# Kernel optimization log

Hardware: AMD Instinct MI355X
Metric: run time of the kernel (lower is better)

The kernel has to match this reference:

```python
import jax, jax.numpy as jnp
import numpy as np

N_NODES = 100000
N_EDGES = 1200000
MAX_ATOM_TYPE = 100
NUM_FEATURES = 92
GC_DIM = 64          # pre_layer_dim == gc_dim == CGConv channels
NUM_RBF = 32
NUM_GC_LAYERS = 4
CUTOFF_UPPER = 5.0
BN_EPS = 1e-5


def setup_inputs() -> dict:
    key = jax.random.key(0)
    ks = jax.random.split(key, 12)
    atom_types = jax.random.randint(ks[0], (N_NODES,), 0, MAX_ATOM_TYPE, dtype=jnp.int32)
    pos = jax.random.uniform(ks[1], (N_NODES, 3), dtype=jnp.float32) * 6.0  # box side 6 -> many dists < cutoff
    edge_index = jax.random.randint(ks[2], (2, N_EDGES), 0, N_NODES, dtype=jnp.int32)
    # parameters
    emb = jax.random.normal(ks[3], (MAX_ATOM_TYPE, NUM_FEATURES), dtype=jnp.float32)
    s = 1.0 / np.sqrt(NUM_FEATURES)
    pre_W = jax.random.uniform(ks[4], (NUM_FEATURES, GC_DIM), minval=-s, maxval=s, dtype=jnp.float32)
    pre_b = jnp.zeros((GC_DIM,), jnp.float32)
    zdim = 2 * GC_DIM + NUM_RBF  # [x_i, x_j, edge_attr]
    sz = 1.0 / np.sqrt(zdim)
    Wf = jax.random.uniform(ks[5], (NUM_GC_LAYERS, zdim, GC_DIM), minval=-sz, maxval=sz, dtype=jnp.float32)
    bf = jnp.zeros((NUM_GC_LAYERS, GC_DIM), jnp.float32)
    Ws = jax.random.uniform(ks[6], (NUM_GC_LAYERS, zdim, GC_DIM), minval=-sz, maxval=sz, dtype=jnp.float32)
    bs = jnp.zeros((NUM_GC_LAYERS, GC_DIM), jnp.float32)
    bn_gamma = jnp.ones((NUM_GC_LAYERS, GC_DIM), jnp.float32)
    bn_beta = jnp.zeros((NUM_GC_LAYERS, GC_DIM), jnp.float32)
    # ExpNormalSmearing (torchmd-net) init
    start = np.exp(-CUTOFF_UPPER)
    means = jnp.asarray(np.linspace(start, 1.0, NUM_RBF), jnp.float32)
    betas = jnp.full((NUM_RBF,), (2.0 / NUM_RBF * (1.0 - start)) ** -2, jnp.float32)
    return {"atom_types": atom_types, "pos": pos, "edge_index": edge_index,
            "emb": emb, "pre_W": pre_W, "pre_b": pre_b,
            "Wf": Wf, "bf": bf, "Ws": Ws, "bs": bs,
            "bn_gamma": bn_gamma, "bn_beta": bn_beta,
            "means": means, "betas": betas}


def _forward(atom_types, pos, edge_index, emb, pre_W, pre_b, Wf, bf, Ws, bs,
             bn_gamma, bn_beta, means, betas):
    src, dst = edge_index[0], edge_index[1]
    # distance (edge_vec = pos[src] - pos[dst])
    vec = pos[src] - pos[dst]                                  # [E,3]
    dist = jnp.sqrt(jnp.sum(vec * vec, axis=-1) + 1e-12)       # [E]
    # expnorm RBF with cosine cutoff (cutoff_lower = 0)
    cutoff = 0.5 * (jnp.cos(dist * (np.pi / CUTOFF_UPPER)) + 1.0) * (dist < CUTOFF_UPPER)
    alpha = 5.0 / CUTOFF_UPPER
    edge_attr = cutoff[:, None] * jnp.exp(
        -betas * (jnp.exp(-alpha * dist)[:, None] - means) ** 2)  # [E,NUM_RBF]
    # embedding + pre layer
    x = emb[atom_types]                                        # [N,F]
    x = jax.nn.relu(x @ pre_W + pre_b)                         # [N,C]
    # mean-aggregation degree (scatter-mean denominator)
    deg = jax.ops.segment_sum(jnp.ones_like(dist), dst, num_segments=N_NODES)
    inv_deg = jnp.where(deg > 0, 1.0 / jnp.maximum(deg, 1.0), 0.0)[:, None]
    for l in range(NUM_GC_LAYERS):
        # CGConv: z = [x_i, x_j, e]; out = x + mean_j(sigmoid(lin_f(z)) * softplus(lin_s(z)))
        z = jnp.concatenate([x[dst], x[src], edge_attr], axis=-1)   # [E, 2C+R]
        msg = jax.nn.sigmoid(z @ Wf[l] + bf[l]) * jax.nn.softplus(z @ Ws[l] + bs[l])
        agg = jax.ops.segment_sum(msg, dst, num_segments=N_NODES) * inv_deg
        x = x + agg
        # BatchNorm1d (batch statistics, biased var, as in torch training mode)
        mu = jnp.mean(x, axis=0)
        var = jnp.mean((x - mu) ** 2, axis=0)
        x = (x - mu) * jax.lax.rsqrt(var + BN_EPS) * bn_gamma[l] + bn_beta[l]
    return x


def reference(atom_types, pos, edge_index, emb, pre_W, pre_b, Wf, bf, Ws, bs,
              bn_gamma, bn_beta, means, betas):
    return _forward(atom_types, pos, edge_index, emb, pre_W, pre_b, Wf, bf, Ws, bs,
                    bn_gamma, bn_beta, means, betas)
```

## Files before the change

### kernel.cpp

```cpp
#include <hip/hip_runtime.h>
#include <math.h>

#define N_NODES 100000
#define N_EDGES 1200000
#define GC 64
#define RBF 32
#define NLAYERS 4
#define NF 92
#define NATOM 100
#define BN_EPS 1e-5f
#define TILE_GRID 2048
#define NWIN (N_EDGES / 16)
#define LOG2E 1.44269504f
#define LN2 0.69314718f

typedef _Float16 half8 __attribute__((ext_vector_type(8)));
typedef _Float16 half4 __attribute__((ext_vector_type(4)));
typedef _Float16 half2v __attribute__((ext_vector_type(2)));
typedef float f32x4 __attribute__((ext_vector_type(4)));
union U32H2 { unsigned int u; half2v h; };

__global__ __launch_bounds__(256) void deg_kernel(
    const int* __restrict__ ei, int* __restrict__ deg)
{
    int e = blockIdx.x * 256 + threadIdx.x;
    if (e >= N_EDGES) return;
    atomicAdd(&deg[ei[N_EDGES + e]], 1);
}

__global__ __launch_bounds__(256) void scan_a_kernel(const int* __restrict__ deg, int* __restrict__ bsums)
{
    __shared__ int sm[256];
    int tid = threadIdx.x;
    int i = blockIdx.x * 256 + tid;
    int v = (i < N_NODES) ? deg[i] : 0;
    sm[tid] = v;
    __syncthreads();
    for (int s = 128; s > 0; s >>= 1) {
        if (tid < s) sm[tid] += sm[tid + s];
        __syncthreads();
    }
    if (tid == 0) bsums[blockIdx.x] = sm[0];
}

__global__ __launch_bounds__(512) void scan_b_kernel(const int* __restrict__ bsums, int* __restrict__ boffs)
{
    __shared__ int sm[512];
    int tid = threadIdx.x;
    int v = (tid < 391) ? bsums[tid] : 0;
    sm[tid] = v;
    __syncthreads();
    for (int off = 1; off < 512; off <<= 1) {
        int t = (tid >= off) ? sm[tid - off] : 0;
        __syncthreads();
        sm[tid] += t;
        __syncthreads();
    }
    boffs[tid] = (tid == 0) ? 0 : sm[tid - 1];
}

__global__ __launch_bounds__(256) void scan_c_kernel(
    const int* __restrict__ deg, const int* __restrict__ boffs,
    int* __restrict__ row_st, float* __restrict__ inv_deg)
{
    __shared__ int sm[256];
    int tid = threadIdx.x;
    int i = blockIdx.x * 256 + tid;
    int v = (i < N_NODES) ? deg[i] : 0;
    sm[tid] = v;
    __syncthreads();
    for (int off = 1; off < 256; off <<= 1) {
        int t = (tid >= off) ? sm[tid - off] : 0;
        __syncthreads();
        sm[tid] += t;
        __syncthreads();
    }
    if (i <= N_NODES) row_st[i] = boffs[blockIdx.x] + sm[tid] - v;
    if (i < N_NODES) inv_deg[i] = (v > 0) ? (1.0f / (float)v) : 0.0f;
}

__global__ __launch_bounds__(256) void scatter_perm_kernel(
    const int* __restrict__ ei, const int* __restrict__ row_st,
    int* __restrict__ cursor, int2* __restrict__ csr_sd)
{
    int e = blockIdx.x * 256 + threadIdx.x;
    if (e >= N_EDGES) return;
    int s = ei[e];
    int d = ei[N_EDGES + e];
    int p = atomicAdd(&cursor[d], 1);
    csr_sd[row_st[d] + p] = make_int2(s, d);
}

__global__ __launch_bounds__(256) void edge_post_kernel(
    const int2* __restrict__ csr_sd, const float* __restrict__ pos,
    const float* __restrict__ inv_deg,
    const float* __restrict__ means, const float* __restrict__ betas,
    int* __restrict__ csr_src, int* __restrict__ csr_dst,
    unsigned int* __restrict__ ea,
    unsigned char* __restrict__ seg8, int* __restrict__ wnode,
    _Float16* __restrict__ inv_e)
{
    __shared__ int sdst[256];
    int t = blockIdx.x * 256 + threadIdx.x;
    if (t < N_EDGES) {
        int2 v = csr_sd[t];
        int s = v.x, d = v.y;
        csr_src[t] = s;
        csr_dst[t] = d;
        sdst[threadIdx.x] = d;
        inv_e[t] = (_Float16)(inv_deg[d] * LN2);

        float dx = pos[s * 3 + 0] - pos[d * 3 + 0];
        float dy = pos[s * 3 + 1] - pos[d * 3 + 1];
        float dz = pos[s * 3 + 2] - pos[d * 3 + 2];
        float dist = sqrtf(dx * dx + dy * dy + dz * dz + 1e-12f);
        float cut = 0.0f;
        if (dist < 5.0f) cut = 0.5f * (__cosf(dist * 0.6283185307179586f) + 1.0f);
        float ex = __expf(-dist);
        union { _Float16 h[32]; uint4 u[4]; } pk;
#pragma unroll
        for (int k = 0; k < 32; k++) {
            float vk = ex - means[k];
            pk.h[k] = (_Float16)(cut * __expf(-betas[k] * vk * vk));
        }
        uint4* op = (uint4*)(ea + (size_t)t * 16);
        op[0] = pk.u[0];
        op[1] = pk.u[1];
        op[2] = pk.u[2];
        op[3] = pk.u[3];
    }
    __syncthreads();
    if (threadIdx.x < 16) {
        int w0 = blockIdx.x * 16 + threadIdx.x;
        if ((size_t)w0 * 16 < N_EDGES) {
            int lb = threadIdx.x * 16;
            int gb = w0 * 16;
            int prev = -1, sg = -1;
            for (int k = 0; k < 16; k++) {
                int dd = sdst[lb + k];
                if (dd != prev) { sg++; prev = dd; wnode[gb + sg] = dd; }
                seg8[gb + k] = (unsigned char)sg;
            }
            for (int m = sg + 1; m < 16; m++) wnode[gb + m] = -1;
        }
    }
}

__global__ __launch_bounds__(256) void prep_const_kernel(
    const float* __restrict__ Wf, const float* __restrict__ Ws,
    _Float16* __restrict__ wf16, _Float16* __restrict__ ws16,
    const float* __restrict__ emb, const float* __restrict__ pre_W,
    const float* __restrict__ pre_b, float* __restrict__ T)
{
    int b = blockIdx.x;
    if (b < 160) {
        int i = b * 256 + threadIdx.x;
        int l = i / (160 * GC);
        int r = i - l * 160 * GC;
        int k = r >> 6;
        int col = r & 63;
        size_t o = ((size_t)l * GC + col) * 160 + k;
        wf16[o] = (_Float16)(Wf[i] * LOG2E);
        ws16[o] = (_Float16)(Ws[i] * LOG2E);
    } else {
        int a = (b - 160) * 4 + (threadIdx.x >> 6);
        int c = threadIdx.x & 63;
        if (a < NATOM) {
            float acc = pre_b[c];
            for (int k = 0; k < NF; k++) acc = fmaf(emb[a * NF + k], pre_W[k * GC + c], acc);
            T[a * GC + c] = fmaxf(acc, 0.0f);
        }
    }
}

static __device__ __forceinline__ void proj_mfma16(
    const _Float16* __restrict__ wf, const _Float16* __restrict__ ws,
    const float* __restrict__ bfv, const float* __restrict__ bsv,
    const half8 Bn[2], int cb, int node, unsigned int* __restrict__ P2u)
{
    const int lane = threadIdx.x & 63;
    const int quad = lane >> 4;
    const int r16 = lane & 15;
    f32x4 accf[2], accs[2];
#pragma unroll
    for (int sub = 0; sub < 2; sub++) {
        accf[sub] = (f32x4){0.f, 0.f, 0.f, 0.f};
        accs[sub] = (f32x4){0.f, 0.f, 0.f, 0.f};
    }
#pragma unroll
    for (int kt = 0; kt < 2; kt++) {
#pragma unroll
        for (int sub = 0; sub < 2; sub++) {
            int chan = cb + sub * 16 + r16;
            half8 a = *(const half8*)(wf + (size_t)chan * 160 + kt * 32 + quad * 8);
            half8 b = *(const half8*)(ws + (size_t)chan * 160 + kt * 32 + quad * 8);
            accf[sub] = __builtin_amdgcn_mfma_f32_16x16x32_f16(a, Bn[kt], accf[sub], 0, 0, 0);
            accs[sub] = __builtin_amdgcn_mfma_f32_16x16x32_f16(b, Bn[kt], accs[sub], 0, 0, 0);
        }
    }
#pragma unroll
    for (int sub = 0; sub < 2; sub++) {
        float4 bf4 = *(const float4*)(bfv + cb + sub * 16 + quad * 4);
        float4 bs4 = *(const float4*)(bsv + cb + sub * 16 + quad * 4);
        half8 h = { (_Float16)(accf[sub][0] + bf4.x * LOG2E), (_Float16)(accs[sub][0] + bs4.x * LOG2E),
                    (_Float16)(accf[sub][1] + bf4.y * LOG2E), (_Float16)(accs[sub][1] + bs4.y * LOG2E),
                    (_Float16)(accf[sub][2] + bf4.z * LOG2E), (_Float16)(accs[sub][2] + bs4.z * LOG2E),
                    (_Float16)(accf[sub][3] + bf4.w * LOG2E), (_Float16)(accs[sub][3] + bs4.w * LOG2E) };
        *(half8*)(P2u + (size_t)node * GC + cb + sub * 16 + quad * 4) = h;
    }
}

__global__ __launch_bounds__(256) void initproj_kernel(
    const int* __restrict__ atom_types, const float* __restrict__ T,
    float* __restrict__ x, _Float16* __restrict__ x16,
    const _Float16* __restrict__ wf, const _Float16* __restrict__ ws,
    const float* __restrict__ bfv, const float* __restrict__ bsv,
    unsigned int* __restrict__ P2u)
{
    __shared__ _Float16 lx[32 * 72];
    const int nb = blockIdx.x * 32;

#pragma unroll
    for (int rep = 0; rep < 2; rep++) {
        int g = rep * 256 + threadIdx.x;
        int gi = blockIdx.x * 512 + g;
        int node = g >> 4;
        int c4 = (g & 15) * 4;
        int a = atom_types[nb + node];
        float4 v = ((const float4*)T)[a * 16 + (g & 15)];
        ((float4*)x)[gi] = v;
        half4 h = { (_Float16)v.x, (_Float16)v.y, (_Float16)v.z, (_Float16)v.w };
        ((half4*)x16)[gi] = h;
        *(half4*)(lx + node * 72 + c4) = h;
    }
    __syncthreads();

    const int lane = threadIdx.x & 63;
    const int wid = threadIdx.x >> 6;
    const int quad = lane >> 4;
    const int r16 = lane & 15;
    const int cb = (wid & 1) * 32;
    const int tn = (wid >> 1) * 16 + r16;
    half8 Bn[2];
    Bn[0] = *(const half8*)(lx + tn * 72 + quad * 8);
    Bn[1] = *(const half8*)(lx + tn * 72 + 32 + quad * 8);
    proj_mfma16(wf, ws, bfv, bsv, Bn, cb, nb + tn, P2u);
}

__global__ __launch_bounds__(256) void bnproj_kernel(
    const float* __restrict__ xn, const float* __restrict__ stats,
    const float* __restrict__ gamma, const float* __restrict__ beta,
    float* __restrict__ xout, _Float16* __restrict__ x16,
    const _Float16* __restrict__ wf, const _Float16* __restrict__ ws,
    const float* __restrict__ bfv, const float* __restrict__ bsv,
    unsigned int* __restrict__ P2u)
{
    __shared__ _Float16 lx[32 * 72];
    const int nb = blockIdx.x * 32;
    const float invN = 1.0f / (float)N_NODES;

#pragma unroll
    for (int rep = 0; rep < 2; rep++) {
        int g = rep * 256 + threadIdx.x;
        int gi = blockIdx.x * 512 + g;
        int node = g >> 4;
        int c4 = (g & 15) * 4;
        float4 v = ((const float4*)xn)[gi];
        float vv[4] = {v.x, v.y, v.z, v.w};
        float o[4];
#pragma unroll
        for (int t = 0; t < 4; t++) {
            int c = c4 + t;
            float mu = stats[c] * invN;
            float var = stats[64 + c] * invN - mu * mu;
            float sc = gamma[c] * rsqrtf(var + BN_EPS);
            o[t] = (vv[t] - mu) * sc + beta[c];
        }
        ((float4*)xout)[gi] = make_float4(o[0], o[1], o[2], o[3]);
        half4 h = { (_Float16)o[0], (_Float16)o[1], (_Float16)o[2], (_Float16)o[3] };
        ((half4*)x16)[gi] = h;
        *(half4*)(lx + node * 72 + c4) = h;
    }
    __syncthreads();

    const int lane = threadIdx.x & 63;
    const int wid = threadIdx.x >> 6;
    const int quad = lane >> 4;
    const int r16 = lane & 15;
    const int cb = (wid & 1) * 32;
    const int tn = (wid >> 1) * 16 + r16;
    half8 Bn[2];
    Bn[0] = *(const half8*)(lx + tn * 72 + quad * 8);
    Bn[1] = *(const half8*)(lx + tn * 72 + 32 + quad * 8);
    proj_mfma16(wf, ws, bfv, bsv, Bn, cb, nb + tn, P2u);
}

static __device__ __forceinline__ void compute_win(
    half8 S0, half8 S1, half8 E, int4 d4, int moff,
    const half8 (&WGF)[3][2], const half8 (&WGS)[3][2],
    int r16, int quad, int cb,
    const unsigned char* __restrict__ seg8, const int* __restrict__ wnode,
    const _Float16* __restrict__ inv_e, const unsigned int* __restrict__ P2u,
    float* __restrict__ x)
{
    unsigned int pv0, pv1, pv2, pv3, pv4, pv5, pv6, pv7;
    {
        const unsigned int* p0 = P2u + (size_t)d4.x * GC + cb + r16;
        const unsigned int* p1 = P2u + (size_t)d4.y * GC + cb + r16;
        const unsigned int* p2 = P2u + (size_t)d4.z * GC + cb + r16;
        const unsigned int* p3 = P2u + (size_t)d4.w * GC + cb + r16;
        pv0 = p0[0];  pv4 = p0[16];
        pv1 = p1[0];  pv5 = p1[16];
        pv2 = p2[0];  pv6 = p2[16];
        pv3 = p3[0];  pv7 = p3[16];
    }
    unsigned int segq = *(const unsigned int*)(seg8 + moff + quad * 4);
    int4 wn4 = *(const int4*)(wnode + moff + quad * 4);
    half4 inv4 = *(const half4*)(inv_e + moff + quad * 4);

    const f32x4 zf = (f32x4){0.0f, 0.0f, 0.0f, 0.0f};
    f32x4 accf[2], accs[2];
    __builtin_amdgcn_s_setprio(1);
#pragma unroll
    for (int ctl = 0; ctl < 2; ctl++) {
        accf[ctl] = __builtin_amdgcn_mfma_f32_16x16x32_f16(S0, WGF[0][ctl], zf, 0, 0, 0);
        accs[ctl] = __builtin_amdgcn_mfma_f32_16x16x32_f16(S0, WGS[0][ctl], zf, 0, 0, 0);
        accf[ctl] = __builtin_amdgcn_mfma_f32_16x16x32_f16(S1, WGF[1][ctl], accf[ctl], 0, 0, 0);
        accs[ctl] = __builtin_amdgcn_mfma_f32_16x16x32_f16(S1, WGS[1][ctl], accs[ctl], 0, 0, 0);
        accf[ctl] = __builtin_amdgcn_mfma_f32_16x16x32_f16(E,  WGF[2][ctl], accf[ctl], 0, 0, 0);
        accs[ctl] = __builtin_amdgcn_mfma_f32_16x16x32_f16(E,  WGS[2][ctl], accs[ctl], 0, 0, 0);
    }
    __builtin_amdgcn_s_setprio(0);

    unsigned int pvv[8] = {pv0, pv1, pv2, pv3, pv4, pv5, pv6, pv7};
    half4 msgh[2];
#pragma unroll
    for (int ctl = 0; ctl < 2; ctl++) {
#pragma unroll
        for (int rr = 0; rr < 4; rr++) {
            U32H2 t; t.u = pvv[ctl * 4 + rr];
            float af = accf[ctl][rr] + (float)t.h.x;
            float as = accs[ctl][rr] + (float)t.h.y;
            float sg = __builtin_amdgcn_rcpf(1.0f + __builtin_amdgcn_exp2f(-af));
            float sp = __builtin_amdgcn_logf(1.0f + __builtin_amdgcn_exp2f(as));
            msgh[ctl][rr] = (_Float16)(sg * sp);
        }
    }
    half4 am;
#pragma unroll
    for (int j = 0; j < 4; j++) {
        int sj = (segq >> (8 * j)) & 0xff;
        am[j] = (sj == r16) ? inv4[j] : (_Float16)0.0f;
    }
    int wa[4] = { wn4.x, wn4.y, wn4.z, wn4.w };
#pragma unroll
    for (int ctl = 0; ctl < 2; ctl++) {
        f32x4 red = __builtin_amdgcn_mfma_f32_16x16x16f16(am, msgh[ctl], zf, 0, 0, 0);
#pragma unroll
        for (int rr = 0; rr < 4; rr++) {
            int nd = wa[rr];
            if (nd >= 0) atomicAdd(&x[(size_t)nd * GC + cb + ctl * 16 + r16], red[rr]);
        }
    }
}

#define LOADSET(S0_, S1_, EE_, SRC_, WW_)                                            \
    S0_ = *(const half8*)(x16 + (size_t)(SRC_) * GC + quad * 8);                     \
    S1_ = *(const half8*)(x16 + (size_t)(SRC_) * GC + 32 + quad * 8);                \
    EE_ = *(const half8*)(ea + ((size_t)(WW_) * 16 + r16) * RBF + quad * 8);

__global__ __launch_bounds__(256, 3) void win_mfma_kernel(
    const _Float16* __restrict__ x16, const _Float16* __restrict__ ea,
    const int* __restrict__ csr_src, const int* __restrict__ csr_dst,
    const unsigned char* __restrict__ seg8, const int* __restrict__ wnode,
    const _Float16* __restrict__ inv_e, const unsigned int* __restrict__ P2u,
    const _Float16* __restrict__ wf16, const _Float16* __restrict__ ws16,
    float* __restrict__ x)
{
    const int lane = threadIdx.x & 63;
    const int wid = __builtin_amdgcn_readfirstlane(threadIdx.x >> 6);
    const int quad = lane >> 4;
    const int r16 = lane & 15;
    const int wgid = blockIdx.x * 4 + wid;
    const int cb = (wgid & 1) * 32;
    int w = wgid >> 1;
    const int NSEQ = TILE_GRID * 2;

    half8 WGF[3][2], WGS[3][2];
#pragma unroll
    for (int ctl = 0; ctl < 2; ctl++) {
        const _Float16* wfp = wf16 + (size_t)(cb + ctl * 16 + r16) * 160 + 64 + quad * 8;
        const _Float16* wsp = ws16 + (size_t)(cb + ctl * 16 + r16) * 160 + 64 + quad * 8;
#pragma unroll
        for (int kt = 0; kt < 3; kt++) {
            WGF[kt][ctl] = *(const half8*)(wfp + kt * 32);
            WGS[kt][ctl] = *(const half8*)(wsp + kt * 32);
        }
    }

    half8 AS0, AS1, AE, BS0, BS1, BE, CS0, CS1, CE;
    int4 d4A, d4B, d4C;
    int moffA, moffB, moffC;
    {
        int s_ = csr_src[w * 16 + r16];
        d4A = *(const int4*)(csr_dst + w * 16 + quad * 4);
        LOADSET(AS0, AS1, AE, s_, w);
        moffA = w * 16;
    }
    {
        int wB = w + NSEQ; if (wB >= NWIN) wB = NWIN - 1;
        int s_ = csr_src[wB * 16 + r16];
        d4B = *(const int4*)(csr_dst + wB * 16 + quad * 4);
        LOADSET(BS0, BS1, BE, s_, wB);
        moffB = wB * 16;
    }
    {
        int wCx = w + 2 * NSEQ; if (wCx >= NWIN) wCx = NWIN - 1;
        int s_ = csr_src[wCx * 16 + r16];
        d4C = *(const int4*)(csr_dst + wCx * 16 + quad * 4);
        LOADSET(CS0, CS1, CE, s_, wCx);
        moffC = wCx * 16;
    }
    int wD = w + 3 * NSEQ; if (wD >= NWIN) wD = NWIN - 1;
    int sD = csr_src[wD * 16 + r16];
    int4 d4D = *(const int4*)(csr_dst + wD * 16 + quad * 4);

    while (true) {
        compute_win(AS0, AS1, AE, d4A, moffA,
                    WGF, WGS, r16, quad, cb, seg8, wnode, inv_e, P2u, x);
        LOADSET(AS0, AS1, AE, sD, wD);
        d4A = d4D; moffA = wD * 16;
        wD += NSEQ; if (wD >= NWIN) wD = NWIN - 1;
        sD = csr_src[wD * 16 + r16];
        d4D = *(const int4*)(csr_dst + wD * 16 + quad * 4);
        w += NSEQ;
        if (w >= NWIN) break;

        compute_win(BS0, BS1, BE, d4B, moffB,
                    WGF, WGS, r16, quad, cb, seg8, wnode, inv_e, P2u, x);
        LOADSET(BS0, BS1, BE, sD, wD);
        d4B = d4D; moffB = wD * 16;
        wD += NSEQ; if (wD >= NWIN) wD = NWIN - 1;
        sD = csr_src[wD * 16 + r16];
        d4D = *(const int4*)(csr_dst + wD * 16 + quad * 4);
        w += NSEQ;
        if (w >= NWIN) break;

        compute_win(CS0, CS1, CE, d4C, moffC,
                    WGF, WGS, r16, quad, cb, seg8, wnode, inv_e, P2u, x);
        LOADSET(CS0, CS1, CE, sD, wD);
        d4C = d4D; moffC = wD * 16;
        wD += NSEQ; if (wD >= NWIN) wD = NWIN - 1;
        sD = csr_src[wD * 16 + r16];
        d4D = *(const int4*)(csr_dst + wD * 16 + quad * 4);
        w += NSEQ;
        if (w >= NWIN) break;
    }
}

__global__ __launch_bounds__(256) void stats_kernel(const float* __restrict__ x, float* __restrict__ stats)
{
    const int lane = threadIdx.x & 63;
    const int wid = threadIdx.x >> 6;
    int w = blockIdx.x * 4 + wid;
    float s1 = 0.0f, s2 = 0.0f;
    for (int n = w; n < N_NODES; n += 2048) {
        float v = x[(size_t)n * GC + lane];
        s1 += v;
        s2 = fmaf(v, v, s2);
    }
    __shared__ float rs1[4][64];
    __shared__ float rs2[4][64];
    rs1[wid][lane] = s1;
    rs2[wid][lane] = s2;
    __syncthreads();
    if (threadIdx.x < 64) {
        atomicAdd(&stats[lane], rs1[0][lane] + rs1[1][lane] + rs1[2][lane] + rs1[3][lane]);
    } else if (threadIdx.x < 128) {
        int c = threadIdx.x & 63;
        atomicAdd(&stats[64 + c], rs2[0][c] + rs2[1][c] + rs2[2][c] + rs2[3][c]);
    }
}

__global__ __launch_bounds__(256) void bn_kernel(
    const float* __restrict__ xn, const float* __restrict__ stats,
    const float* __restrict__ gamma, const float* __restrict__ beta,
    float* __restrict__ out)
{
    int i = blockIdx.x * 256 + threadIdx.x;
    int c4 = (i & 15) * 4;
    float4 v = ((const float4*)xn)[i];
    float vv[4] = {v.x, v.y, v.z, v.w};
    float o[4];
    const float invN = 1.0f / (float)N_NODES;
#pragma unroll
    for (int t = 0; t < 4; t++) {
        int c = c4 + t;
        float mu = stats[c] * invN;
        float var = stats[64 + c] * invN - mu * mu;
        float sc = gamma[c] * rsqrtf(var + BN_EPS);
        o[t] = (vv[t] - mu) * sc + beta[c];
    }
    ((float4*)out)[i] = make_float4(o[0], o[1], o[2], o[3]);
}

extern "C" void kernel_launch(void* const* d_in, const int* in_sizes, int n_in,
                              void* d_out, int out_size, void* d_ws, size_t ws_size,
                              hipStream_t stream)
{
    const int* atom_types = (const int*)d_in[0];
    const float* pos = (const float*)d_in[1];
    const int* edge_index = (const int*)d_in[2];
    const float* emb = (const float*)d_in[3];
    const float* pre_W = (const float*)d_in[4];
    const float* pre_b = (const float*)d_in[5];
    const float* Wf = (const float*)d_in[6];
    const float* bf = (const float*)d_in[7];
    const float* Ws = (const float*)d_in[8];
    const float* bs = (const float*)d_in[9];
    const float* gamma = (const float*)d_in[10];
    const float* beta = (const float*)d_in[11];
    const float* means = (const float*)d_in[12];
    const float* betas = (const float*)d_in[13];

    char* base = (char*)d_ws;
    char* p = base;
    auto alloc = [&](size_t bytes) -> char* {
        char* r = p;
        p += (bytes + 255) & ~(size_t)255;
        return r;
    };
    unsigned int* ea = (unsigned int*)alloc((size_t)N_EDGES * RBF * 2);
    float* x = (float*)alloc((size_t)N_NODES * GC * 4);
    _Float16* x16 = (_Float16*)alloc((size_t)N_NODES * GC * 2);
    unsigned int* P2u = (unsigned int*)alloc((size_t)N_NODES * GC * 4);
    int2* csr_sd = (int2*)alloc((size_t)N_EDGES * 8);
    int* csr_src = (int*)alloc((size_t)N_EDGES * 4);
    int* csr_dst = (int*)alloc((size_t)N_EDGES * 4);
    int* wnode = (int*)alloc((size_t)N_EDGES * 4);
    unsigned char* seg8 = (unsigned char*)alloc((size_t)N_EDGES);
    _Float16* inv_e = (_Float16*)alloc((size_t)N_EDGES * 2);
    _Float16* wf16 = (_Float16*)alloc((size_t)NLAYERS * GC * 160 * 2);
    _Float16* ws16 = (_Float16*)alloc((size_t)NLAYERS * GC * 160 * 2);
    int* row_st = (int*)alloc((size_t)(N_NODES + 1) * 4);
    float* inv_deg = (float*)alloc((size_t)N_NODES * 4);
    float* T = (float*)alloc((size_t)NATOM * GC * 4);
    int* bsums = (int*)alloc(512 * 4);
    int* boffs = (int*)alloc(512 * 4);
    const size_t ZR_INTS = (size_t)2 * N_NODES + 128 * NLAYERS + 64;
    char* zr = alloc(ZR_INTS * 4);
    int* deg = (int*)zr;
    int* cursor = deg + N_NODES;
    float* stats = (float*)(cursor + N_NODES);

    if ((size_t)(p - base) > ws_size) return;

    (void)hipMemsetAsync(zr, 0, ZR_INTS * 4, stream);

    const int EG = (N_EDGES + 255) / 256;
    deg_kernel<<<EG, 256, 0, stream>>>(edge_index, deg);
    scan_a_kernel<<<391, 256, 0, stream>>>(deg, bsums);
    scan_b_kernel<<<1, 512, 0, stream>>>(bsums, boffs);
    scan_c_kernel<<<391, 256, 0, stream>>>(deg, boffs, row_st, inv_deg);
    scatter_perm_kernel<<<EG, 256, 0, stream>>>(edge_index, row_st, cursor, csr_sd);
    edge_post_kernel<<<EG, 256, 0, stream>>>(csr_sd, pos, inv_deg, means, betas,
                                             csr_src, csr_dst, ea, seg8, wnode, inv_e);
    prep_const_kernel<<<185, 256, 0, stream>>>(Wf, Ws, wf16, ws16, emb, pre_W, pre_b, T);
    initproj_kernel<<<N_NODES / 32, 256, 0, stream>>>(atom_types, T, x, x16,
                                                      wf16, ws16, bf, bs, P2u);

    for (int l = 0; l < NLAYERS; l++) {
        win_mfma_kernel<<<TILE_GRID, 256, 0, stream>>>(
            x16, (const _Float16*)ea, csr_src, csr_dst, seg8, wnode, inv_e, P2u,
            wf16 + (size_t)l * GC * 160, ws16 + (size_t)l * GC * 160, x);
        stats_kernel<<<512, 256, 0, stream>>>(x, stats + l * 128);
        if (l < NLAYERS - 1) {
            bnproj_kernel<<<N_NODES / 32, 256, 0, stream>>>(
                x, stats + l * 128, gamma + l * GC, beta + l * GC, x, x16,
                wf16 + (size_t)(l + 1) * GC * 160, ws16 + (size_t)(l + 1) * GC * 160,
                bf + (l + 1) * GC, bs + (l + 1) * GC, P2u);
        } else {
            bn_kernel<<<N_NODES * 16 / 256, 256, 0, stream>>>(
                x, stats + l * 128, gamma + l * GC, beta + l * GC, (float*)d_out);
        }
    }
}
```

Baseline: 801.0 us.

## Capture atomic rank in degree pass, fold block-offset scan, use nontemporal loads

The degree kernel now records each edge's atomic return value as its rank within its destination. The scatter step then places edges directly into csr_src/csr_dst with no second atomic pass and no intermediate int2 buffer. The separate single-block offset scan is removed; each scan_c block sums its preceding block totals itself. Streaming edge data in the main message-passing kernel (ea, csr indices, seg8, wnode, inv_e) is read with nontemporal loads so it does not push reused node data out of cache. Costs are an extra rank array and redundant prefix reductions in every scan block.

```diff
diff --git a/kernel.cpp b/kernel.cpp
--- a/kernel.cpp
+++ b/kernel.cpp
@@ -18,14 +18,15 @@
 typedef _Float16 half4 __attribute__((ext_vector_type(4)));
 typedef _Float16 half2v __attribute__((ext_vector_type(2)));
 typedef float f32x4 __attribute__((ext_vector_type(4)));
+typedef int i32x4 __attribute__((ext_vector_type(4)));
 union U32H2 { unsigned int u; half2v h; };
 
-__global__ __launch_bounds__(256) void deg_kernel(
-    const int* __restrict__ ei, int* __restrict__ deg)
+__global__ __launch_bounds__(256) void degrank_kernel(
+    const int* __restrict__ ei, int* __restrict__ deg, int* __restrict__ rank)
 {
     int e = blockIdx.x * 256 + threadIdx.x;
     if (e >= N_EDGES) return;
-    atomicAdd(&deg[ei[N_EDGES + e]], 1);
+    rank[e] = atomicAdd(&deg[ei[N_EDGES + e]], 1);
 }
 
 __global__ __launch_bounds__(256) void scan_a_kernel(const int* __restrict__ deg, int* __restrict__ bsums)
@@ -43,28 +44,24 @@
     if (tid == 0) bsums[blockIdx.x] = sm[0];
 }
 
-__global__ __launch_bounds__(512) void scan_b_kernel(const int* __restrict__ bsums, int* __restrict__ boffs)
-{
-    __shared__ int sm[512];
-    int tid = threadIdx.x;
-    int v = (tid < 391) ? bsums[tid] : 0;
-    sm[tid] = v;
-    __syncthreads();
-    for (int off = 1; off < 512; off <<= 1) {
-        int t = (tid >= off) ? sm[tid - off] : 0;
-        __syncthreads();
-        sm[tid] += t;
-        __syncthreads();
-    }
-    boffs[tid] = (tid == 0) ? 0 : sm[tid - 1];
-}
-
 __global__ __launch_bounds__(256) void scan_c_kernel(
-    const int* __restrict__ deg, const int* __restrict__ boffs,
+    const int* __restrict__ deg, const int* __restrict__ bsums,
     int* __restrict__ row_st, float* __restrict__ inv_deg)
 {
     __shared__ int sm[256];
     int tid = threadIdx.x;
+    int acc = 0;
+    if (tid < blockIdx.x) acc = bsums[tid];
+    int t2 = tid + 256;
+    if (t2 < blockIdx.x) acc += bsums[t2];
+    sm[tid] = acc;
+    __syncthreads();
+    for (int s = 128; s > 0; s >>= 1) {
+        if (tid < s) sm[tid] += sm[tid + s];
+        __syncthreads();
+    }
+    int boff = sm[0];
+    __syncthreads();
     int i = blockIdx.x * 256 + tid;
     int v = (i < N_NODES) ? deg[i] : 0;
     sm[tid] = v;
@@ -75,27 +72,27 @@
         sm[tid] += t;
         __syncthreads();
     }
-    if (i <= N_NODES) row_st[i] = boffs[blockIdx.x] + sm[tid] - v;
+    if (i <= N_NODES) row_st[i] = boff + sm[tid] - v;
     if (i < N_NODES) inv_deg[i] = (v > 0) ? (1.0f / (float)v) : 0.0f;
 }
 
 __global__ __launch_bounds__(256) void scatter_perm_kernel(
     const int* __restrict__ ei, const int* __restrict__ row_st,
-    int* __restrict__ cursor, int2* __restrict__ csr_sd)
+    const int* __restrict__ rank, int* __restrict__ csr_src, int* __restrict__ csr_dst)
 {
     int e = blockIdx.x * 256 + threadIdx.x;
     if (e >= N_EDGES) return;
     int s = ei[e];
     int d = ei[N_EDGES + e];
-    int p = atomicAdd(&cursor[d], 1);
-    csr_sd[row_st[d] + p] = make_int2(s, d);
+    int idx = row_st[d] + rank[e];
+    csr_src[idx] = s;
+    csr_dst[idx] = d;
 }
 
 __global__ __launch_bounds__(256) void edge_post_kernel(
-    const int2* __restrict__ csr_sd, const float* __restrict__ pos,
-    const float* __restrict__ inv_deg,
+    const int* __restrict__ csr_src, const int* __restrict__ csr_dst,
+    const float* __restrict__ pos, const float* __restrict__ inv_deg,
     const float* __restrict__ means, const float* __restrict__ betas,
-    int* __restrict__ csr_src, int* __restrict__ csr_dst,
     unsigned int* __restrict__ ea,
     unsigned char* __restrict__ seg8, int* __restrict__ wnode,
     _Float16* __restrict__ inv_e)
@@ -103,10 +100,8 @@
     __shared__ int sdst[256];
     int t = blockIdx.x * 256 + threadIdx.x;
     if (t < N_EDGES) {
-        int2 v = csr_sd[t];
-        int s = v.x, d = v.y;
-        csr_src[t] = s;
-        csr_dst[t] = d;
+        int s = csr_src[t];
+        int d = csr_dst[t];
         sdst[threadIdx.x] = d;
         inv_e[t] = (_Float16)(inv_deg[d] * LN2);
 
@@ -296,7 +291,7 @@
 }
 
 static __device__ __forceinline__ void compute_win(
-    half8 S0, half8 S1, half8 E, int4 d4, int moff,
+    half8 S0, half8 S1, half8 E, i32x4 d4, int moff,
     const half8 (&WGF)[3][2], const half8 (&WGS)[3][2],
     int r16, int quad, int cb,
     const unsigned char* __restrict__ seg8, const int* __restrict__ wnode,
@@ -305,18 +300,18 @@
 {
     unsigned int pv0, pv1, pv2, pv3, pv4, pv5, pv6, pv7;
     {
-        const unsigned int* p0 = P2u + (size_t)d4.x * GC + cb + r16;
-        const unsigned int* p1 = P2u + (size_t)d4.y * GC + cb + r16;
-        const unsigned int* p2 = P2u + (size_t)d4.z * GC + cb + r16;
-        const unsigned int* p3 = P2u + (size_t)d4.w * GC + cb + r16;
+        const unsigned int* p0 = P2u + (size_t)d4[0] * GC + cb + r16;
+        const unsigned int* p1 = P2u + (size_t)d4[1] * GC + cb + r16;
+        const unsigned int* p2 = P2u + (size_t)d4[2] * GC + cb + r16;
+        const unsigned int* p3 = P2u + (size_t)d4[3] * GC + cb + r16;
         pv0 = p0[0];  pv4 = p0[16];
         pv1 = p1[0];  pv5 = p1[16];
         pv2 = p2[0];  pv6 = p2[16];
         pv3 = p3[0];  pv7 = p3[16];
     }
-    unsigned int segq = *(const unsigned int*)(seg8 + moff + quad * 4);
-    int4 wn4 = *(const int4*)(wnode + moff + quad * 4);
-    half4 inv4 = *(const half4*)(inv_e + moff + quad * 4);
+    unsigned int segq = __builtin_nontemporal_load((const unsigned int*)(seg8 + moff + quad * 4));
+    i32x4 wn4 = __builtin_nontemporal_load((const i32x4*)(wnode + moff + quad * 4));
+    half4 inv4 = __builtin_nontemporal_load((const half4*)(inv_e + moff + quad * 4));
 
     const f32x4 zf = (f32x4){0.0f, 0.0f, 0.0f, 0.0f};
     f32x4 accf[2], accs[2];
@@ -352,13 +347,12 @@
         int sj = (segq >> (8 * j)) & 0xff;
         am[j] = (sj == r16) ? inv4[j] : (_Float16)0.0f;
     }
-    int wa[4] = { wn4.x, wn4.y, wn4.z, wn4.w };
 #pragma unroll
     for (int ctl = 0; ctl < 2; ctl++) {
         f32x4 red = __builtin_amdgcn_mfma_f32_16x16x16f16(am, msgh[ctl], zf, 0, 0, 0);
 #pragma unroll
         for (int rr = 0; rr < 4; rr++) {
-            int nd = wa[rr];
+            int nd = wn4[rr];
             if (nd >= 0) atomicAdd(&x[(size_t)nd * GC + cb + ctl * 16 + r16], red[rr]);
         }
     }
@@ -367,7 +361,7 @@
 #define LOADSET(S0_, S1_, EE_, SRC_, WW_)                                            \
     S0_ = *(const half8*)(x16 + (size_t)(SRC_) * GC + quad * 8);                     \
     S1_ = *(const half8*)(x16 + (size_t)(SRC_) * GC + 32 + quad * 8);                \
-    EE_ = *(const half8*)(ea + ((size_t)(WW_) * 16 + r16) * RBF + quad * 8);
+    EE_ = __builtin_nontemporal_load((const half8*)(ea + ((size_t)(WW_) * 16 + r16) * RBF + quad * 8));
 
 __global__ __launch_bounds__(256, 3) void win_mfma_kernel(
     const _Float16* __restrict__ x16, const _Float16* __restrict__ ea,
@@ -399,31 +393,31 @@
     }
 
     half8 AS0, AS1, AE, BS0, BS1, BE, CS0, CS1, CE;
-    int4 d4A, d4B, d4C;
+    i32x4 d4A, d4B, d4C;
     int moffA, moffB, moffC;
     {
-        int s_ = csr_src[w * 16 + r16];
-        d4A = *(const int4*)(csr_dst + w * 16 + quad * 4);
+        int s_ = __builtin_nontemporal_load(csr_src + w * 16 + r16);
+        d4A = __builtin_nontemporal_load((const i32x4*)(csr_dst + w * 16 + quad * 4));
         LOADSET(AS0, AS1, AE, s_, w);
         moffA = w * 16;
     }
     {
         int wB = w + NSEQ; if (wB >= NWIN) wB = NWIN - 1;
-        int s_ = csr_src[wB * 16 + r16];
-        d4B = *(const int4*)(csr_dst + wB * 16 + quad * 4);
+        int s_ = __builtin_nontemporal_load(csr_src + wB * 16 + r16);
+        d4B = __builtin_nontemporal_load((const i32x4*)(csr_dst + wB * 16 + quad * 4));
         LOADSET(BS0, BS1, BE, s_, wB);
         moffB = wB * 16;
     }
     {
         int wCx = w + 2 * NSEQ; if (wCx >= NWIN) wCx = NWIN - 1;
-        int s_ = csr_src[wCx * 16 + r16];
-        d4C = *(const int4*)(csr_dst + wCx * 16 + quad * 4);
+        int s_ = __builtin_nontemporal_load(csr_src + wCx * 16 + r16);
+        d4C = __builtin_nontemporal_load((const i32x4*)(csr_dst + wCx * 16 + quad * 4));
         LOADSET(CS0, CS1, CE, s_, wCx);
         moffC = wCx * 16;
     }
     int wD = w + 3 * NSEQ; if (wD >= NWIN) wD = NWIN - 1;
-    int sD = csr_src[wD * 16 + r16];
-    int4 d4D = *(const int4*)(csr_dst + wD * 16 + quad * 4);
+    int sD = __builtin_nontemporal_load(csr_src + wD * 16 + r16);
+    i32x4 d4D = __builtin_nontemporal_load((const i32x4*)(csr_dst + wD * 16 + quad * 4));
 
     while (true) {
         compute_win(AS0, AS1, AE, d4A, moffA,
@@ -431,8 +425,8 @@
         LOADSET(AS0, AS1, AE, sD, wD);
         d4A = d4D; moffA = wD * 16;
         wD += NSEQ; if (wD >= NWIN) wD = NWIN - 1;
-        sD = csr_src[wD * 16 + r16];
-        d4D = *(const int4*)(csr_dst + wD * 16 + quad * 4);
+        sD = __builtin_nontemporal_load(csr_src + wD * 16 + r16);
+        d4D = __builtin_nontemporal_load((const i32x4*)(csr_dst + wD * 16 + quad * 4));
         w += NSEQ;
         if (w >= NWIN) break;
 
@@ -441,8 +435,8 @@
         LOADSET(BS0, BS1, BE, sD, wD);
         d4B = d4D; moffB = wD * 16;
         wD += NSEQ; if (wD >= NWIN) wD = NWIN - 1;
-        sD = csr_src[wD * 16 + r16];
-        d4D = *(const int4*)(csr_dst + wD * 16 + quad * 4);
+        sD = __builtin_nontemporal_load(csr_src + wD * 16 + r16);
+        d4D = __builtin_nontemporal_load((const i32x4*)(csr_dst + wD * 16 + quad * 4));
         w += NSEQ;
         if (w >= NWIN) break;
 
@@ -451,8 +445,8 @@
         LOADSET(CS0, CS1, CE, sD, wD);
         d4C = d4D; moffC = wD * 16;
         wD += NSEQ; if (wD >= NWIN) wD = NWIN - 1;
-        sD = csr_src[wD * 16 + r16];
-        d4D = *(const int4*)(csr_dst + wD * 16 + quad * 4);
+        sD = __builtin_nontemporal_load(csr_src + wD * 16 + r16);
+        d4D = __builtin_nontemporal_load((const i32x4*)(csr_dst + wD * 16 + quad * 4));
         w += NSEQ;
         if (w >= NWIN) break;
     }
@@ -534,9 +528,9 @@
     float* x = (float*)alloc((size_t)N_NODES * GC * 4);
     _Float16* x16 = (_Float16*)alloc((size_t)N_NODES * GC * 2);
     unsigned int* P2u = (unsigned int*)alloc((size_t)N_NODES * GC * 4);
-    int2* csr_sd = (int2*)alloc((size_t)N_EDGES * 8);
     int* csr_src = (int*)alloc((size_t)N_EDGES * 4);
     int* csr_dst = (int*)alloc((size_t)N_EDGES * 4);
+    int* rank = (int*)alloc((size_t)N_EDGES * 4);
     int* wnode = (int*)alloc((size_t)N_EDGES * 4);
     unsigned char* seg8 = (unsigned char*)alloc((size_t)N_EDGES);
     _Float16* inv_e = (_Float16*)alloc((size_t)N_EDGES * 2);
@@ -546,25 +540,22 @@
     float* inv_deg = (float*)alloc((size_t)N_NODES * 4);
     float* T = (float*)alloc((size_t)NATOM * GC * 4);
     int* bsums = (int*)alloc(512 * 4);
-    int* boffs = (int*)alloc(512 * 4);
-    const size_t ZR_INTS = (size_t)2 * N_NODES + 128 * NLAYERS + 64;
+    const size_t ZR_INTS = (size_t)N_NODES + 128 * NLAYERS + 64;
     char* zr = alloc(ZR_INTS * 4);
     int* deg = (int*)zr;
-    int* cursor = deg + N_NODES;
-    float* stats = (float*)(cursor + N_NODES);
+    float* stats = (float*)(deg + N_NODES);
 
     if ((size_t)(p - base) > ws_size) return;
 
     (void)hipMemsetAsync(zr, 0, ZR_INTS * 4, stream);
 
     const int EG = (N_EDGES + 255) / 256;
-    deg_kernel<<<EG, 256, 0, stream>>>(edge_index, deg);
+    degrank_kernel<<<EG, 256, 0, stream>>>(edge_index, deg, rank);
     scan_a_kernel<<<391, 256, 0, stream>>>(deg, bsums);
-    scan_b_kernel<<<1, 512, 0, stream>>>(bsums, boffs);
-    scan_c_kernel<<<391, 256, 0, stream>>>(deg, boffs, row_st, inv_deg);
-    scatter_perm_kernel<<<EG, 256, 0, stream>>>(edge_index, row_st, cursor, csr_sd);
-    edge_post_kernel<<<EG, 256, 0, stream>>>(csr_sd, pos, inv_deg, means, betas,
-                                             csr_src, csr_dst, ea, seg8, wnode, inv_e);
+    scan_c_kernel<<<391, 256, 0, stream>>>(deg, bsums, row_st, inv_deg);
+    scatter_perm_kernel<<<EG, 256, 0, stream>>>(edge_index, row_st, rank, csr_src, csr_dst);
+    edge_post_kernel<<<EG, 256, 0, stream>>>(csr_src, csr_dst, pos, inv_deg, means, betas,
+                                             ea, seg8, wnode, inv_e);
     prep_const_kernel<<<185, 256, 0, stream>>>(Wf, Ws, wf16, ws16, emb, pre_W, pre_b, T);
     initproj_kernel<<<N_NODES / 32, 256, 0, stream>>>(atom_types, T, x, x16,
                                                       wf16, ws16, bf, bs, P2u);
```

Measured after the change: 818.0 us. +2.1%, slower.
